# Kernel tuning notes

Measured on AMD Instinct MI355X. Metric: run time of the kernel, lower is better.

Reference implementation:

```python
import jax, jax.numpy as jnp
import numpy as np

L = 16384
D = 1000


def setup_inputs() -> dict:
    key = jax.random.key(0)
    ks = jax.random.split(key, 7)
    x = jax.random.normal(ks[0], (L,), dtype=jnp.float32)
    size = jax.random.normal(ks[1], (D,), dtype=jnp.float32)
    theta = jax.random.normal(ks[2], (D,), dtype=jnp.float32) * (2 * jnp.pi) / 500.0
    # eqx.nn.Linear-style params (uniform init scale is irrelevant for correctness; use scaled normal)
    W1 = jax.random.normal(ks[3], (D, D), dtype=jnp.float32) / jnp.sqrt(D).astype(jnp.float32)
    b1 = jax.random.normal(ks[4], (D,), dtype=jnp.float32) * 0.01
    Wf = jax.random.normal(ks[5], (10, D), dtype=jnp.float32) / jnp.sqrt(D).astype(jnp.float32)
    bf = jax.random.normal(ks[6], (10,), dtype=jnp.float32) * 0.01
    return {"x": x, "size": size, "theta": theta, "W1": W1, "b1": b1, "Wf": Wf, "bf": bf}


def reference(x, size, theta, W1, b1, Wf, bf):
    # x: [L] -> repeat to [L, D]
    x_rep = jnp.broadcast_to(x[:, None], (x.shape[0], size.shape[0]))  # [L, D]
    # diagonal complex decay per channel
    z = jnp.exp(-jnp.exp(size) + 1j * theta)  # [D] complex64

    # linear recurrence v_t = z * v_{t-1} + x_t via associative scan over time axis
    def combine(a, b):
        pa, va = a
        pb, vb = b
        return (pa * pb, va * pb + vb)

    p0 = jnp.broadcast_to(z[None, :], x_rep.shape)  # [L, D]
    v0 = x_rep.astype(z.dtype)                       # [L, D] complex
    _, h = jax.lax.associative_scan(combine, (p0, v0), axis=0)  # [L, D] complex

    # per-timestep Linear(D, D) on complex states (real weights), residual, relu of real part
    y = h @ W1.T + b1            # complex [L, D]
    x1 = jax.nn.relu(jnp.real(y + x_rep))  # [L, D] real

    # final Linear(D, 10) on last timestep, softmax
    logits = x1[-1] @ Wf.T + bf  # [10]
    return jax.nn.softmax(logits)
```

## Files before the change

### kernel.cpp

```cpp
#include <hip/hip_runtime.h>
#include <math.h>

#define LSEQ 16384
#define DCH  1000

__global__ __launch_bounds__(256) void scan_last_kernel(
    const float* __restrict__ x, const float* __restrict__ sz,
    const float* __restrict__ th, float* __restrict__ u) {
  const int d = blockIdx.x;
  const int tid = threadIdx.x;

  const float r = expf(-expf(sz[d]));
  const float zr = r * cosf(th[d]);
  const float zi = r * sinf(th[d]);

  const float* xp = x + tid * 64;
  float pr = 1.f, pi = 0.f;
  float vr = 0.f, vi = 0.f;

#pragma unroll
  for (int j4 = 0; j4 < 16; ++j4) {
    float4 xv4 = reinterpret_cast<const float4*>(xp)[j4];
    float xs[4] = {xv4.x, xv4.y, xv4.z, xv4.w};
#pragma unroll
    for (int k = 0; k < 4; ++k) {
      float xv = xs[k];
      float nvr = fmaf(zr, vr, fmaf(-zi, vi, xv));
      float nvi = fmaf(zr, vi, zi * vr);
      vr = nvr; vi = nvi;
      float npr = fmaf(zr, pr, -zi * pi);
      float npi = fmaf(zr, pi, zi * pr);
      pr = npr; pi = npi;
    }
  }

  const int lane = tid & 63;
  for (int o = 1; o < 64; o <<= 1) {
    float opr = __shfl_down(pr, o);
    float opi = __shfl_down(pi, o);
    float ovr = __shfl_down(vr, o);
    float ovi = __shfl_down(vi, o);
    if (lane + o < 64) {
      float nvr = vr * opr - vi * opi + ovr;
      float nvi = vr * opi + vi * opr + ovi;
      float npr = pr * opr - pi * opi;
      float npi = pr * opi + pi * opr;
      vr = nvr; vi = nvi; pr = npr; pi = npi;
    }
  }

  __shared__ float spr[4], spi[4], svr[4], svi[4];
  const int w = tid >> 6;
  if (lane == 0) { spr[w] = pr; spi[w] = pi; svr[w] = vr; svi[w] = vi; }
  __syncthreads();
  if (tid == 0) {
    float Pr = spr[0], Pi = spi[0], Vr = svr[0], Vi = svi[0];
#pragma unroll
    for (int k = 1; k < 4; ++k) {
      float opr = spr[k], opi = spi[k], ovr = svr[k], ovi = svi[k];
      float nVr = Vr * opr - Vi * opi + ovr;
      float nVi = Vr * opi + Vi * opr + ovi;
      Vr = nVr; Vi = nVi;
      float nPr = Pr * opr - Pi * opi;
      float nPi = Pr * opi + Pi * opr;
      Pr = nPr; Pi = nPi;
    }
    u[d] = Vr;
  }
}

__global__ __launch_bounds__(256) void mv_relu_kernel(
    const float* __restrict__ u, const float* __restrict__ W1,
    const float* __restrict__ b1, const float* __restrict__ x,
    float* __restrict__ x1) {
  const int j = blockIdx.x;
  const int tid = threadIdx.x;
  const float* wrow = W1 + (size_t)j * DCH;
  float acc = 0.f;
  for (int dd = tid; dd < DCH; dd += 256) acc = fmaf(u[dd], wrow[dd], acc);
  for (int o = 32; o > 0; o >>= 1) acc += __shfl_down(acc, o);
  __shared__ float s[4];
  const int lane = tid & 63, w = tid >> 6;
  if (lane == 0) s[w] = acc;
  __syncthreads();
  if (tid == 0) {
    float t = s[0] + s[1] + s[2] + s[3];
    x1[j] = fmaxf(t + b1[j] + x[LSEQ - 1], 0.f);
  }
}

__global__ __launch_bounds__(256) void head_softmax_kernel(
    const float* __restrict__ x1, const float* __restrict__ Wf,
    const float* __restrict__ bf, float* __restrict__ out) {
  const int tid = threadIdx.x;
  float part[10];
#pragma unroll
  for (int i = 0; i < 10; ++i) part[i] = 0.f;
  for (int dd = tid; dd < DCH; dd += 256) {
    float xv = x1[dd];
#pragma unroll
    for (int i = 0; i < 10; ++i) part[i] = fmaf(xv, Wf[i * DCH + dd], part[i]);
  }
#pragma unroll
  for (int i = 0; i < 10; ++i)
    for (int o = 32; o > 0; o >>= 1) part[i] += __shfl_down(part[i], o);

  __shared__ float s[4][10];
  const int lane = tid & 63, w = tid >> 6;
  if (lane == 0) {
#pragma unroll
    for (int i = 0; i < 10; ++i) s[w][i] = part[i];
  }
  __syncthreads();
  if (tid == 0) {
    float logits[10];
    float m = -1e30f;
#pragma unroll
    for (int i = 0; i < 10; ++i) {
      logits[i] = s[0][i] + s[1][i] + s[2][i] + s[3][i] + bf[i];
      m = fmaxf(m, logits[i]);
    }
    float ssum = 0.f;
#pragma unroll
    for (int i = 0; i < 10; ++i) { logits[i] = expf(logits[i] - m); ssum += logits[i]; }
    float inv = 1.f / ssum;
#pragma unroll
    for (int i = 0; i < 10; ++i) out[i] = logits[i] * inv;
  }
}

extern "C" void kernel_launch(void* const* d_in, const int* in_sizes, int n_in,
                              void* d_out, int out_size, void* d_ws, size_t ws_size,
                              hipStream_t stream) {
  const float* x  = (const float*)d_in[0];
  const float* sz = (const float*)d_in[1];
  const float* th = (const float*)d_in[2];
  const float* W1 = (const float*)d_in[3];
  const float* b1 = (const float*)d_in[4];
  const float* Wf = (const float*)d_in[5];
  const float* bf = (const float*)d_in[6];
  float* out = (float*)d_out;

  float* u  = (float*)d_ws;
  float* x1 = u + 1024;

  scan_last_kernel<<<DCH, 256, 0, stream>>>(x, sz, th, u);
  mv_relu_kernel<<<DCH, 256, 0, stream>>>(u, W1, b1, x, x1);
  head_softmax_kernel<<<1, 256, 0, stream>>>(x1, Wf, bf, out);
}
```

Before: 86.95 us.

## Fuse scan, matvec and softmax head into one cooperative kernel

Replaces three kernel launches with one cooperative kernel of 256 blocks that use grid-wide syncs between the stages. Each thread keeps its 64 inputs in registers and reuses them across several channels. The scan combine is replaced by a direct weighted sum: each thread's partial state is multiplied by z^(64*(255-tid)), computed by repeated squaring, and the block reduces the results. The matvec uses float4 loads with u staged in shared memory. This removes launch gaps and the shuffle-scan overhead, at the cost of grid-sync latency and fewer blocks doing the scan work.

```diff
diff --git a/kernel.cpp b/kernel.cpp
--- a/kernel.cpp
+++ b/kernel.cpp
@@ -1,131 +1,151 @@
 #include <hip/hip_runtime.h>
+#include <hip/hip_cooperative_groups.h>
 #include <math.h>
+
+namespace cg = cooperative_groups;
 
 #define LSEQ 16384
 #define DCH  1000
+#define NBLK 256
 
-__global__ __launch_bounds__(256) void scan_last_kernel(
+__global__ __launch_bounds__(256) void fused_kernel(
     const float* __restrict__ x, const float* __restrict__ sz,
-    const float* __restrict__ th, float* __restrict__ u) {
-  const int d = blockIdx.x;
+    const float* __restrict__ th, const float* __restrict__ W1,
+    const float* __restrict__ b1, const float* __restrict__ Wf,
+    const float* __restrict__ bf, float* __restrict__ out,
+    float* __restrict__ u, float* __restrict__ x1) {
   const int tid = threadIdx.x;
+  const int bid = blockIdx.x;
+  const int lane = tid & 63;
+  const int w = tid >> 6;
+  cg::grid_group grid = cg::this_grid();
 
-  const float r = expf(-expf(sz[d]));
-  const float zr = r * cosf(th[d]);
-  const float zi = r * sinf(th[d]);
+  __shared__ float sred[4];
+  __shared__ float uL[1000];
+  __shared__ float sredB[4][4];
+  __shared__ float sH[4][10];
 
-  const float* xp = x + tid * 64;
-  float pr = 1.f, pi = 0.f;
-  float vr = 0.f, vi = 0.f;
+  float xr0[64];
+  {
+    const float4* xp4 = reinterpret_cast<const float4*>(x + tid * 64);
+#pragma unroll
+    for (int m = 0; m < 16; ++m) {
+      float4 v4 = xp4[m];
+      xr0[4 * m + 0] = v4.x; xr0[4 * m + 1] = v4.y;
+      xr0[4 * m + 2] = v4.z; xr0[4 * m + 3] = v4.w;
+    }
+  }
 
+  for (int d = bid; d < DCH; d += NBLK) {
+    const float r  = expf(-expf(sz[d]));
+    const float tv = th[d];
+    const float zr = r * cosf(tv);
+    const float zi = r * sinf(tv);
+
+    float vr = 0.f, vi = 0.f;
 #pragma unroll
-  for (int j4 = 0; j4 < 16; ++j4) {
-    float4 xv4 = reinterpret_cast<const float4*>(xp)[j4];
-    float xs[4] = {xv4.x, xv4.y, xv4.z, xv4.w};
-#pragma unroll
-    for (int k = 0; k < 4; ++k) {
-      float xv = xs[k];
+    for (int k = 0; k < 64; ++k) {
+      float xv = xr0[k];
       float nvr = fmaf(zr, vr, fmaf(-zi, vi, xv));
       float nvi = fmaf(zr, vi, zi * vr);
       vr = nvr; vi = nvi;
-      float npr = fmaf(zr, pr, -zi * pi);
-      float npi = fmaf(zr, pi, zi * pr);
-      pr = npr; pi = npi;
+    }
+
+    float br = zr, bi = zi;
+#pragma unroll
+    for (int k = 0; k < 6; ++k) { float t = br * br - bi * bi; bi = 2.f * br * bi; br = t; }
+    float wr = 1.f, wi = 0.f;
+    const int e = 255 - tid;
+#pragma unroll
+    for (int k = 0; k < 8; ++k) {
+      float nr = wr * br - wi * bi;
+      float ni = wr * bi + wi * br;
+      bool bit = (e >> k) & 1;
+      wr = bit ? nr : wr;
+      wi = bit ? ni : wi;
+      if (k < 7) { float t = br * br - bi * bi; bi = 2.f * br * bi; br = t; }
+    }
+
+    float s = wr * vr - wi * vi;
+#pragma unroll
+    for (int o = 32; o > 0; o >>= 1) s += __shfl_xor(s, o);
+    if (lane == 0) sred[w] = s;
+    __syncthreads();
+    if (tid == 0) u[d] = sred[0] + sred[1] + sred[2] + sred[3];
+    __syncthreads();
+  }
+
+  grid.sync();
+
+  const float xlast = x[LSEQ - 1];
+  if (tid < 250) reinterpret_cast<float4*>(uL)[tid] = reinterpret_cast<const float4*>(u)[tid];
+  __syncthreads();
+
+  float accs[4] = {0.f, 0.f, 0.f, 0.f};
+#pragma unroll
+  for (int k = 0; k < 4; ++k) {
+    const int j = bid + NBLK * k;
+    if (j < DCH && tid < 250) {
+      const float4* wrow = reinterpret_cast<const float4*>(W1 + (size_t)j * DCH);
+      float4 w4 = wrow[tid];
+      float4 u4 = reinterpret_cast<const float4*>(uL)[tid];
+      accs[k] = fmaf(w4.x, u4.x, fmaf(w4.y, u4.y, fmaf(w4.z, u4.z, w4.w * u4.w)));
+    }
+  }
+#pragma unroll
+  for (int k = 0; k < 4; ++k) {
+#pragma unroll
+    for (int o = 32; o > 0; o >>= 1) accs[k] += __shfl_xor(accs[k], o);
+  }
+  if (lane == 0) {
+#pragma unroll
+    for (int k = 0; k < 4; ++k) sredB[k][w] = accs[k];
+  }
+  __syncthreads();
+  if (tid < 4) {
+    const int j = bid + NBLK * tid;
+    if (j < DCH) {
+      float t = sredB[tid][0] + sredB[tid][1] + sredB[tid][2] + sredB[tid][3];
+      x1[j] = fmaxf(t + b1[j] + xlast, 0.f);
     }
   }
 
-  const int lane = tid & 63;
-  for (int o = 1; o < 64; o <<= 1) {
-    float opr = __shfl_down(pr, o);
-    float opi = __shfl_down(pi, o);
-    float ovr = __shfl_down(vr, o);
-    float ovi = __shfl_down(vi, o);
-    if (lane + o < 64) {
-      float nvr = vr * opr - vi * opi + ovr;
-      float nvi = vr * opi + vi * opr + ovi;
-      float npr = pr * opr - pi * opi;
-      float npi = pr * opi + pi * opr;
-      vr = nvr; vi = nvi; pr = npr; pi = npi;
+  grid.sync();
+
+  if (bid == 0) {
+    float part[10];
+#pragma unroll
+    for (int i = 0; i < 10; ++i) part[i] = 0.f;
+    for (int dd = tid; dd < DCH; dd += 256) {
+      float xv = x1[dd];
+#pragma unroll
+      for (int i = 0; i < 10; ++i) part[i] = fmaf(xv, Wf[i * DCH + dd], part[i]);
     }
-  }
-
-  __shared__ float spr[4], spi[4], svr[4], svi[4];
-  const int w = tid >> 6;
-  if (lane == 0) { spr[w] = pr; spi[w] = pi; svr[w] = vr; svi[w] = vi; }
-  __syncthreads();
-  if (tid == 0) {
-    float Pr = spr[0], Pi = spi[0], Vr = svr[0], Vi = svi[0];
-#pragma unroll
-    for (int k = 1; k < 4; ++k) {
-      float opr = spr[k], opi = spi[k], ovr = svr[k], ovi = svi[k];
-      float nVr = Vr * opr - Vi * opi + ovr;
-      float nVi = Vr * opi + Vi * opr + ovi;
-      Vr = nVr; Vi = nVi;
-      float nPr = Pr * opr - Pi * opi;
-      float nPi = Pr * opi + Pi * opr;
-      Pr = nPr; Pi = nPi;
-    }
-    u[d] = Vr;
-  }
-}
-
-__global__ __launch_bounds__(256) void mv_relu_kernel(
-    const float* __restrict__ u, const float* __restrict__ W1,
-    const float* __restrict__ b1, const float* __restrict__ x,
-    float* __restrict__ x1) {
-  const int j = blockIdx.x;
-  const int tid = threadIdx.x;
-  const float* wrow = W1 + (size_t)j * DCH;
-  float acc = 0.f;
-  for (int dd = tid; dd < DCH; dd += 256) acc = fmaf(u[dd], wrow[dd], acc);
-  for (int o = 32; o > 0; o >>= 1) acc += __shfl_down(acc, o);
-  __shared__ float s[4];
-  const int lane = tid & 63, w = tid >> 6;
-  if (lane == 0) s[w] = acc;
-  __syncthreads();
-  if (tid == 0) {
-    float t = s[0] + s[1] + s[2] + s[3];
-    x1[j] = fmaxf(t + b1[j] + x[LSEQ - 1], 0.f);
-  }
-}
-
-__global__ __launch_bounds__(256) void head_softmax_kernel(
-    const float* __restrict__ x1, const float* __restrict__ Wf,
-    const float* __restrict__ bf, float* __restrict__ out) {
-  const int tid = threadIdx.x;
-  float part[10];
-#pragma unroll
-  for (int i = 0; i < 10; ++i) part[i] = 0.f;
-  for (int dd = tid; dd < DCH; dd += 256) {
-    float xv = x1[dd];
-#pragma unroll
-    for (int i = 0; i < 10; ++i) part[i] = fmaf(xv, Wf[i * DCH + dd], part[i]);
-  }
-#pragma unroll
-  for (int i = 0; i < 10; ++i)
-    for (int o = 32; o > 0; o >>= 1) part[i] += __shfl_down(part[i], o);
-
-  __shared__ float s[4][10];
-  const int lane = tid & 63, w = tid >> 6;
-  if (lane == 0) {
-#pragma unroll
-    for (int i = 0; i < 10; ++i) s[w][i] = part[i];
-  }
-  __syncthreads();
-  if (tid == 0) {
-    float logits[10];
-    float m = -1e30f;
 #pragma unroll
     for (int i = 0; i < 10; ++i) {
-      logits[i] = s[0][i] + s[1][i] + s[2][i] + s[3][i] + bf[i];
-      m = fmaxf(m, logits[i]);
+#pragma unroll
+      for (int o = 32; o > 0; o >>= 1) part[i] += __shfl_xor(part[i], o);
     }
-    float ssum = 0.f;
+    if (lane == 0) {
 #pragma unroll
-    for (int i = 0; i < 10; ++i) { logits[i] = expf(logits[i] - m); ssum += logits[i]; }
-    float inv = 1.f / ssum;
+      for (int i = 0; i < 10; ++i) sH[w][i] = part[i];
+    }
+    __syncthreads();
+    if (tid == 0) {
+      float logits[10];
+      float m = -1e30f;
 #pragma unroll
-    for (int i = 0; i < 10; ++i) out[i] = logits[i] * inv;
+      for (int i = 0; i < 10; ++i) {
+        logits[i] = sH[0][i] + sH[1][i] + sH[2][i] + sH[3][i] + bf[i];
+        m = fmaxf(m, logits[i]);
+      }
+      float ssum = 0.f;
+#pragma unroll
+      for (int i = 0; i < 10; ++i) { logits[i] = expf(logits[i] - m); ssum += logits[i]; }
+      float inv = 1.f / ssum;
+#pragma unroll
+      for (int i = 0; i < 10; ++i) out[i] = logits[i] * inv;
+    }
   }
 }
 
@@ -144,7 +164,7 @@
   float* u  = (float*)d_ws;
   float* x1 = u + 1024;
 
-  scan_last_kernel<<<DCH, 256, 0, stream>>>(x, sz, th, u);
-  mv_relu_kernel<<<DCH, 256, 0, stream>>>(u, W1, b1, x, x1);
-  head_softmax_kernel<<<1, 256, 0, stream>>>(x1, Wf, bf, out);
+  void* args[] = {(void*)&x, (void*)&sz, (void*)&th, (void*)&W1, (void*)&b1,
+                  (void*)&Wf, (void*)&bf, (void*)&out, (void*)&u, (void*)&x1};
+  hipLaunchCooperativeKernel((void*)fused_kernel, dim3(NBLK), dim3(256), args, 0, stream);
 }
```

Result: slower. 143.8 us (+65.3%).
